# Kernel optimization log

Hardware: AMD Instinct MI355X
Metric: run time of the kernel (lower is better)

## Reference

```python
import jax, jax.numpy as jnp
import numpy as np

B, T, D, W, H = 8, 2048, 1024, 16, 8
HD = D // H  # head dim = 128
EPS = 1e-5


def _layernorm(x, g, b):
    m = jnp.mean(x, axis=-1, keepdims=True)
    v = jnp.var(x, axis=-1, keepdims=True)
    return (x - m) / jnp.sqrt(v + EPS) * g + b


def setup_inputs() -> dict:
    key = jax.random.key(0)
    ks = jax.random.split(key, 8)
    s = 0.02
    return {
        "frame_features": jax.random.normal(ks[0], (B, T, D), dtype=jnp.float32),
        "frame_indices": jnp.arange(B * T, dtype=jnp.int64).reshape(B, T),
        # nn.MultiheadAttention packed in-projection (3D, D) and out projection
        "w_qkv": jax.random.normal(ks[1], (3 * D, D), dtype=jnp.float32) * s,
        "b_qkv": jnp.zeros((3 * D,), dtype=jnp.float32),
        "w_out": jax.random.normal(ks[2], (D, D), dtype=jnp.float32) * s,
        "b_out": jnp.zeros((D,), dtype=jnp.float32),
        # FFN: Linear(D, 4D) -> GELU -> Linear(4D, D)
        "w1": jax.random.normal(ks[3], (4 * D, D), dtype=jnp.float32) * s,
        "b1": jnp.zeros((4 * D,), dtype=jnp.float32),
        "w2": jax.random.normal(ks[4], (D, 4 * D), dtype=jnp.float32) * s,
        "b2": jnp.zeros((D,), dtype=jnp.float32),
        "g1": jnp.ones((D,), dtype=jnp.float32),
        "beta1": jnp.zeros((D,), dtype=jnp.float32),
        "g2": jnp.ones((D,), dtype=jnp.float32),
        "beta2": jnp.zeros((D,), dtype=jnp.float32),
    }


def _forward(frame_features, frame_indices, w_qkv, b_qkv, w_out, b_out,
             w1, b1, w2, b2, g1, beta1, g2, beta2):
    # --- sinusoidal temporal positional encoding, indexed by frame number ---
    pos = frame_indices.astype(jnp.float32)[..., None]          # (B, T, 1)
    div = jnp.exp(-jnp.log(10000.0) * jnp.arange(0, D, 2, dtype=jnp.float32) / D)
    ang = pos * div                                              # (B, T, D/2)
    pe = jnp.stack([jnp.sin(ang), jnp.cos(ang)], axis=-1).reshape(B, T, D)
    x = frame_features + pe

    # --- block-diagonal (local window) attention, all windows in one pass ---
    nw = T // W
    xw = x.reshape(B, nw, W, D)
    qkv = jnp.einsum('bnwd,ed->bnwe', xw, w_qkv) + b_qkv         # (B, nw, W, 3D)
    q, k, v = jnp.split(qkv, 3, axis=-1)
    q = q.reshape(B, nw, W, H, HD)
    k = k.reshape(B, nw, W, H, HD)
    v = v.reshape(B, nw, W, H, HD)
    scores = jnp.einsum('bnqhd,bnkhd->bnhqk', q, k) / jnp.sqrt(jnp.float32(HD))
    attn = jax.nn.softmax(scores, axis=-1)
    o = jnp.einsum('bnhqk,bnkhd->bnqhd', attn, v).reshape(B, nw, W, D)
    attn_out = jnp.einsum('bnwd,ed->bnwe', o, w_out) + b_out

    h = _layernorm(xw + attn_out, g1, beta1)
    ffn = jnp.einsum('bnwf,df->bnwd', jax.nn.gelu(
        jnp.einsum('bnwd,fd->bnwf', h, w1) + b1, approximate=False), w2) + b2
    out = _layernorm(h + ffn, g2, beta2)
    return out.reshape(B, T, D)


def reference(frame_features, frame_indices, w_qkv, b_qkv, w_out, b_out,
              w1, b1, w2, b2, g1, beta1, g2, beta2):
    return _forward(frame_features, frame_indices, w_qkv, b_qkv, w_out, b_out,
                    w1, b1, w2, b2, g1, beta1, g2, beta2)
```

## Files before the change

### kernel.cpp

```cpp
#include <hip/hip_runtime.h>
#include <math.h>

typedef __bf16 bf16;
typedef __bf16 bf16x8 __attribute__((ext_vector_type(8)));
typedef __bf16 bf16x4 __attribute__((ext_vector_type(4)));
typedef __bf16 bf16x2 __attribute__((ext_vector_type(2)));
typedef float f32x4 __attribute__((ext_vector_type(4)));

#define ROWS 16384

typedef __attribute__((address_space(3))) void* lds_vp;
typedef const __attribute__((address_space(1))) void* glb_vp;
__device__ __forceinline__ void gload16(const void* g, void* l) {
  __builtin_amdgcn_global_load_lds((glb_vp)g, (lds_vp)l, 16, 0, 0);
}

__global__ __launch_bounds__(256) void cast4_kernel(
    const float* __restrict__ s0, bf16* __restrict__ d0, int n0,
    const float* __restrict__ s1, bf16* __restrict__ d1, int n1,
    const float* __restrict__ s2, bf16* __restrict__ d2, int n2,
    const float* __restrict__ s3, bf16* __restrict__ d3, int n3)
{
  int i = (blockIdx.x * 256 + threadIdx.x) * 8;
  const float* s; bf16* d;
  if (i < n0)                { s = s0; d = d0; }
  else if ((i -= n0) < n1)   { s = s1; d = d1; }
  else if ((i -= n1) < n2)   { s = s2; d = d2; }
  else if ((i -= n2) < n3)   { s = s3; d = d3; }
  else return;
  float4 a = *(const float4*)(s + i);
  float4 b = *(const float4*)(s + i + 4);
  bf16x8 o;
  o[0] = (bf16)a.x; o[1] = (bf16)a.y; o[2] = (bf16)a.z; o[3] = (bf16)a.w;
  o[4] = (bf16)b.x; o[5] = (bf16)b.y; o[6] = (bf16)b.z; o[7] = (bf16)b.w;
  *(bf16x8*)(d + i) = o;
}

__global__ __launch_bounds__(256) void pe_add_kernel(
    const float* __restrict__ ff, const int* __restrict__ idx, bf16* __restrict__ x)
{
  int p   = blockIdx.x * 256 + threadIdx.x;
  int row = p >> 9;
  int j   = p & 511;
  float pos = (float)idx[row];
  float d2  = (float)(2 * j) * (1.0f / 1024.0f);
  float dv  = expf(-9.210340371976184f * d2);
  float ang = pos * dv;
  float s, c;
  sincosf(ang, &s, &c);
  int base = row * 1024 + 2 * j;
  float2 f = *(const float2*)(ff + base);
  bf16x2 o;
  o[0] = (bf16)(f.x + s);
  o[1] = (bf16)(f.y + c);
  *(bf16x2*)(x + base) = o;
}

#define MFMA16 __builtin_amdgcn_mfma_f32_16x16x32_bf16

template<bool GELU, bool RES>
__global__ __launch_bounds__(512, 2) void gemm8(
    const bf16* __restrict__ A, const bf16* __restrict__ Bw,
    const float* __restrict__ bias, const bf16* __restrict__ resid,
    bf16* __restrict__ C, int M, int N, int K)
{
  extern __shared__ char smem[];

  const int tid  = threadIdx.x;
  const int wave = tid >> 6;
  const int lane = tid & 63;
  const int wm = wave >> 2, wn = wave & 3;
  const int ln = lane & 15, q = lane >> 4;
  const int wm8 = wm * 8, wn4 = wn * 4;

  const int nwg = gridDim.x;
  const int nbn = N >> 8;
  const int swz = (blockIdx.x & 7) * (nwg >> 3) + (blockIdx.x >> 3);
  const int bm = (swz / nbn) << 8;
  const int bn = (swz % nbn) << 8;

  const bf16* lA = (const bf16*)smem;
  const int rsw = (ln * 32 + q * 8) ^ (((ln >> 3) & 1) << 4);
  const int raw = wm8 * 512 + rsw;
  const int rbw = 8192 + wn4 * 512 + rsw;

  const int le = lane ^ (((lane >> 5) & 1) << 1);
  const int sr = le >> 2;
  const int sc = (le & 3) * 8;
  const bf16* gAw = A  + (size_t)(bm + wave * 32 + sr) * K + sc;
  const bf16* gBw = Bw + (size_t)(bn + wave * 32 + sr) * K + sc;

#define STAGE_A(BB, KOFF) do { \
    char* _d = smem + (BB) * 32768 + wave * 2048; \
    gload16(gAw + (KOFF), _d); \
    gload16(gAw + 16 * (size_t)K + (KOFF), _d + 1024); } while (0)
#define STAGE_B(BB, KOFF) do { \
    char* _d = smem + (BB) * 32768 + 16384 + wave * 2048; \
    gload16(gBw + (KOFF), _d); \
    gload16(gBw + 16 * (size_t)K + (KOFF), _d + 1024); } while (0)

  f32x4 acc[8][4];
#pragma unroll
  for (int i = 0; i < 8; i++)
#pragma unroll
    for (int j = 0; j < 4; j++) acc[i][j] = {0.f, 0.f, 0.f, 0.f};

  float bv[4];
#pragma unroll
  for (int tn = 0; tn < 4; tn++) bv[tn] = bias[bn + wn * 64 + tn * 16 + ln];

  const int nkt = K >> 5;

  STAGE_A(0, 0);  STAGE_B(0, 0);
  STAGE_A(1, 32); STAGE_B(1, 32);
  STAGE_A(2, 64); STAGE_B(2, 64);
  asm volatile("s_waitcnt vmcnt(8)");
  __builtin_amdgcn_s_barrier();

#define MFROW(T, AF) \
    acc[T][0] = MFMA16(AF, bf0, acc[T][0], 0, 0, 0); \
    acc[T][1] = MFMA16(AF, bf1, acc[T][1], 0, 0, 0); \
    acc[T][2] = MFMA16(AF, bf2, acc[T][2], 0, 0, 0); \
    acc[T][3] = MFMA16(AF, bf3, acc[T][3], 0, 0, 0);

#define KT(B_, KST, STG, VMS) { \
    if (STG) { STAGE_A((((B_) + 3) & 3), (KST)); STAGE_B((((B_) + 3) & 3), (KST)); } \
    const bf16* _pa = lA + (B_) * 16384 + raw; \
    const bf16* _pb = lA + (B_) * 16384 + rbw; \
    bf16x8 af0 = *(const bf16x8*)(_pa); \
    bf16x8 af1 = *(const bf16x8*)(_pa + 512); \
    bf16x8 af2 = *(const bf16x8*)(_pa + 1024); \
    bf16x8 af3 = *(const bf16x8*)(_pa + 1536); \
    bf16x8 af4 = *(const bf16x8*)(_pa + 2048); \
    bf16x8 af5 = *(const bf16x8*)(_pa + 2560); \
    bf16x8 af6 = *(const bf16x8*)(_pa + 3072); \
    bf16x8 af7 = *(const bf16x8*)(_pa + 3584); \
    bf16x8 bf0 = *(const bf16x8*)(_pb); \
    bf16x8 bf1 = *(const bf16x8*)(_pb + 512); \
    bf16x8 bf2 = *(const bf16x8*)(_pb + 1024); \
    bf16x8 bf3 = *(const bf16x8*)(_pb + 1536); \
    __builtin_amdgcn_s_setprio(1); \
    MFROW(0, af0) MFROW(1, af1) MFROW(2, af2) MFROW(3, af3) \
    MFROW(4, af4) MFROW(5, af5) MFROW(6, af6) MFROW(7, af7) \
    __builtin_amdgcn_s_setprio(0); \
    VMS; \
    __builtin_amdgcn_s_barrier(); }

#define V8 asm volatile("s_waitcnt vmcnt(8)")
#define V4 asm volatile("s_waitcnt vmcnt(4)")
#define V0 asm volatile("s_waitcnt vmcnt(0)")
#define VN (void)0

  for (int mm = 0; mm < nkt - 4; mm += 4) {
    const int kst = (mm + 3) * 32;
    KT(0, kst,       true, V8)
    KT(1, kst + 32,  true, V8)
    KT(2, kst + 64,  true, V8)
    KT(3, kst + 96,  true, V8)
  }
  KT(0, (nkt - 1) * 32, true,  V8)
  KT(1, 0,              false, V4)
  KT(2, 0,              false, V0)
  KT(3, 0,              false, VN)
#undef KT
#undef MFROW
#undef V8
#undef V4
#undef V0
#undef VN
#undef STAGE_A
#undef STAGE_B

  bf16* eb = (bf16*)smem;
  const int lrow = tid >> 4;
  const int cb   = (tid & 15) * 16;
#pragma unroll
  for (int tm = 0; tm < 8; tm++) {
    __syncthreads();
#pragma unroll
    for (int tn = 0; tn < 4; tn++)
#pragma unroll
      for (int i = 0; i < 4; i++)
        eb[(wm * 16 + q * 4 + i) * 264 + wn * 64 + tn * 16 + ln] =
            (bf16)(acc[tm][tn][i] + bv[tn]);
    __syncthreads();
    int gR = bm + (lrow >> 4) * 128 + tm * 16 + (lrow & 15);
    size_t rowoff = (size_t)gR * N + bn + cb;
    bf16x8 v0 = *(const bf16x8*)&eb[lrow * 264 + cb];
    bf16x8 v1 = *(const bf16x8*)&eb[lrow * 264 + cb + 8];
    if (RES) {
      bf16x8 r0 = *(const bf16x8*)(resid + rowoff);
      bf16x8 r1 = *(const bf16x8*)(resid + rowoff + 8);
#pragma unroll
      for (int u = 0; u < 8; u++) {
        v0[u] = (bf16)((float)v0[u] + (float)r0[u]);
        v1[u] = (bf16)((float)v1[u] + (float)r1[u]);
      }
    }
    if (GELU) {
#pragma unroll
      for (int u = 0; u < 8; u++) {
        float a = (float)v0[u], c = (float)v1[u];
        float ea = __builtin_amdgcn_exp2f(2.3022082f * a * (1.0f + 0.044715f * a * a));
        float ec = __builtin_amdgcn_exp2f(2.3022082f * c * (1.0f + 0.044715f * c * c));
        v0[u] = (bf16)(a - a * __builtin_amdgcn_rcpf(ea + 1.0f));
        v1[u] = (bf16)(c - c * __builtin_amdgcn_rcpf(ec + 1.0f));
      }
    }
    *(bf16x8*)(C + rowoff)     = v0;
    *(bf16x8*)(C + rowoff + 8) = v1;
  }
}

__global__ __launch_bounds__(256) void attn_kernel(
    const bf16* __restrict__ qkv, bf16* __restrict__ o)
{
  __shared__ bf16 sq[16][136], sk[16][136], sv[16][136];
  __shared__ float ss[16][17];

  int wid = blockIdx.x;
  int h   = wid & 7;
  int win = wid >> 3;
  int tb  = win * 16;

  int t  = threadIdx.x;
  int r  = t >> 4;
  int c8 = (t & 15) * 8;

  const bf16* base = qkv + (size_t)(tb + r) * 3072 + c8;
  *(bf16x8*)&sq[r][c8] = *(const bf16x8*)(base + h * 128);
  *(bf16x8*)&sk[r][c8] = *(const bf16x8*)(base + 1024 + h * 128);
  *(bf16x8*)&sv[r][c8] = *(const bf16x8*)(base + 2048 + h * 128);
  __syncthreads();

  {
    int i = t >> 4, jj = t & 15;
    float s = 0.f;
#pragma unroll
    for (int d8 = 0; d8 < 16; d8++) {
      bf16x8 qa = *(const bf16x8*)&sq[i][d8 * 8];
      bf16x8 kb = *(const bf16x8*)&sk[jj][d8 * 8];
#pragma unroll
      for (int u = 0; u < 8; u++) s += (float)qa[u] * (float)kb[u];
    }
    ss[i][jj] = s * 0.08838834764831845f;
  }
  __syncthreads();

  if (t < 16) {
    float m = -1e30f;
    for (int jj = 0; jj < 16; jj++) m = fmaxf(m, ss[t][jj]);
    float sum = 0.f;
    for (int jj = 0; jj < 16; jj++) { float e = expf(ss[t][jj] - m); ss[t][jj] = e; sum += e; }
    float inv = 1.0f / sum;
    for (int jj = 0; jj < 16; jj++) ss[t][jj] *= inv;
  }
  __syncthreads();

  {
    int i = t >> 4; int d0 = (t & 15) * 8;
    float acc[8] = {0, 0, 0, 0, 0, 0, 0, 0};
#pragma unroll
    for (int jj = 0; jj < 16; jj++) {
      float a = ss[i][jj];
      bf16x8 vv8 = *(const bf16x8*)&sv[jj][d0];
#pragma unroll
      for (int u = 0; u < 8; u++) acc[u] += a * (float)vv8[u];
    }
    bf16* op = o + (size_t)(tb + i) * 1024 + h * 128 + d0;
    bf16x8 ov;
#pragma unroll
    for (int u = 0; u < 8; u++) ov[u] = (bf16)acc[u];
    *(bf16x8*)op = ov;
  }
}

template<typename OUT_T>
__global__ __launch_bounds__(256) void ln_kernel(
    const bf16* __restrict__ x, const float* __restrict__ g,
    const float* __restrict__ b, OUT_T* __restrict__ y)
{
  __shared__ float red[8];
  int row = blockIdx.x;
  int t   = threadIdx.x;
  int lane = t & 63, wave = t >> 6;

  bf16x4 v4 = *(const bf16x4*)(x + (size_t)row * 1024 + t * 4);
  float v[4];
  float s = 0.f, sq = 0.f;
#pragma unroll
  for (int u = 0; u < 4; u++) {
    v[u] = (float)v4[u];
    s += v[u];
    sq += v[u] * v[u];
  }
  for (int off = 32; off > 0; off >>= 1) {
    s  += __shfl_down(s, off);
    sq += __shfl_down(sq, off);
  }
  if (lane == 0) { red[wave * 2] = s; red[wave * 2 + 1] = sq; }
  __syncthreads();
  float st = red[0] + red[2] + red[4] + red[6];
  float qt = red[1] + red[3] + red[5] + red[7];
  float mean = st * (1.0f / 1024.0f);
  float var  = qt * (1.0f / 1024.0f) - mean * mean;
  float inv  = rsqrtf(var + 1e-5f);
  int c = t * 4;
  OUT_T* yr = y + (size_t)row * 1024 + c;
#pragma unroll
  for (int u = 0; u < 4; u++)
    yr[u] = (OUT_T)((v[u] - mean) * inv * g[c + u] + b[c + u]);
}

extern "C" void kernel_launch(void* const* d_in, const int* in_sizes, int n_in,
                              void* d_out, int out_size, void* d_ws, size_t ws_size,
                              hipStream_t stream) {
  const float* ff    = (const float*)d_in[0];
  const int*   idx   = (const int*)d_in[1];
  const float* w_qkv = (const float*)d_in[2];
  const float* b_qkv = (const float*)d_in[3];
  const float* w_out = (const float*)d_in[4];
  const float* b_out = (const float*)d_in[5];
  const float* w1    = (const float*)d_in[6];
  const float* b1    = (const float*)d_in[7];
  const float* w2    = (const float*)d_in[8];
  const float* b2    = (const float*)d_in[9];
  const float* g1    = (const float*)d_in[10];
  const float* be1   = (const float*)d_in[11];
  const float* g2    = (const float*)d_in[12];
  const float* be2   = (const float*)d_in[13];
  float* out = (float*)d_out;

  static bool attrs_done = false;
  if (!attrs_done) {
    attrs_done = true;
    hipFuncSetAttribute(reinterpret_cast<const void*>(&gemm8<false, false>),
                        hipFuncAttributeMaxDynamicSharedMemorySize, 131072);
    hipFuncSetAttribute(reinterpret_cast<const void*>(&gemm8<false, true>),
                        hipFuncAttributeMaxDynamicSharedMemorySize, 131072);
    hipFuncSetAttribute(reinterpret_cast<const void*>(&gemm8<true, false>),
                        hipFuncAttributeMaxDynamicSharedMemorySize, 131072);
  }

  char* p = (char*)d_ws;
  bf16* x_bf = (bf16*)p;  p += (size_t)ROWS * 1024 * 2;
  bf16* big  = (bf16*)p;  p += (size_t)ROWS * 4096 * 2;
  bf16* s_bf = (bf16*)p;  p += (size_t)ROWS * 1024 * 2;
  bf16* h_bf = (bf16*)p;  p += (size_t)ROWS * 1024 * 2;
  bf16* wqb  = (bf16*)p;  p += (size_t)3072 * 1024 * 2;
  bf16* wob  = (bf16*)p;  p += (size_t)1024 * 1024 * 2;
  bf16* w1b  = (bf16*)p;  p += (size_t)4096 * 1024 * 2;
  bf16* w2b  = (bf16*)p;  p += (size_t)1024 * 4096 * 2;
  bf16* o_bf = big + (size_t)ROWS * 3072;
  bf16* g_bf = big;

  cast4_kernel<<<6144, 256, 0, stream>>>(
      w_qkv, wqb, 3072 * 1024,
      w_out, wob, 1024 * 1024,
      w1,    w1b, 4096 * 1024,
      w2,    w2b, 1024 * 4096);

  pe_add_kernel<<<ROWS * 512 / 256, 256, 0, stream>>>(ff, idx, x_bf);

  gemm8<false, false><<<64 * 12, 512, 131072, stream>>>(
      x_bf, wqb, b_qkv, nullptr, big, ROWS, 3072, 1024);
  attn_kernel<<<(ROWS / 16) * 8, 256, 0, stream>>>(big, o_bf);
  gemm8<false, true><<<64 * 4, 512, 131072, stream>>>(
      o_bf, wob, b_out, x_bf, s_bf, ROWS, 1024, 1024);
  ln_kernel<bf16><<<ROWS, 256, 0, stream>>>(s_bf, g1, be1, h_bf);
  gemm8<true, false><<<64 * 16, 512, 131072, stream>>>(
      h_bf, w1b, b1, nullptr, big, ROWS, 4096, 1024);
  gemm8<false, true><<<64 * 4, 512, 131072, stream>>>(
      g_bf, w2b, b2, h_bf, s_bf, ROWS, 1024, 4096);
  ln_kernel<float><<<ROWS, 256, 0, stream>>>(s_bf, g2, be2, out);
}
```

Before: 657.5 us.

## Replace 4-stage LDS pipeline in GEMM with double buffering to halve shared memory

The GEMM main loop moves from a 4-buffer, 3-deep prefetch pipeline to a 2-buffer ping-pong scheme. Each step now waits for all outstanding loads with vmcnt(0) before the barrier. LDS per block drops from 128KB to 64KB, so the launches request 65536 bytes and the max-dynamic-shared-memory attributes are removed. This can let two 512-thread blocks share a CU, at the cost of a shallower prefetch that exposes more global-load latency per k-step.

```diff
diff --git a/kernel.cpp b/kernel.cpp
--- a/kernel.cpp
+++ b/kernel.cpp
@@ -112,9 +112,7 @@
   const int nkt = K >> 5;
 
   STAGE_A(0, 0);  STAGE_B(0, 0);
-  STAGE_A(1, 32); STAGE_B(1, 32);
-  STAGE_A(2, 64); STAGE_B(2, 64);
-  asm volatile("s_waitcnt vmcnt(8)");
+  asm volatile("s_waitcnt vmcnt(0)");
   __builtin_amdgcn_s_barrier();
 
 #define MFROW(T, AF) \
@@ -123,8 +121,9 @@
     acc[T][2] = MFMA16(AF, bf2, acc[T][2], 0, 0, 0); \
     acc[T][3] = MFMA16(AF, bf3, acc[T][3], 0, 0, 0);
 
-#define KT(B_, KST, STG, VMS) { \
-    if (STG) { STAGE_A((((B_) + 3) & 3), (KST)); STAGE_B((((B_) + 3) & 3), (KST)); } \
+#define KT(B_, NEXT) { \
+    const bool stg = (NEXT) < nkt; \
+    if (stg) { STAGE_A((B_) ^ 1, (NEXT) * 32); STAGE_B((B_) ^ 1, (NEXT) * 32); } \
     const bf16* _pa = lA + (B_) * 16384 + raw; \
     const bf16* _pb = lA + (B_) * 16384 + rbw; \
     bf16x8 af0 = *(const bf16x8*)(_pa); \
@@ -143,31 +142,15 @@
     MFROW(0, af0) MFROW(1, af1) MFROW(2, af2) MFROW(3, af3) \
     MFROW(4, af4) MFROW(5, af5) MFROW(6, af6) MFROW(7, af7) \
     __builtin_amdgcn_s_setprio(0); \
-    VMS; \
+    if (stg) { asm volatile("s_waitcnt vmcnt(0)"); } \
     __builtin_amdgcn_s_barrier(); }
 
-#define V8 asm volatile("s_waitcnt vmcnt(8)")
-#define V4 asm volatile("s_waitcnt vmcnt(4)")
-#define V0 asm volatile("s_waitcnt vmcnt(0)")
-#define VN (void)0
-
-  for (int mm = 0; mm < nkt - 4; mm += 4) {
-    const int kst = (mm + 3) * 32;
-    KT(0, kst,       true, V8)
-    KT(1, kst + 32,  true, V8)
-    KT(2, kst + 64,  true, V8)
-    KT(3, kst + 96,  true, V8)
-  }
-  KT(0, (nkt - 1) * 32, true,  V8)
-  KT(1, 0,              false, V4)
-  KT(2, 0,              false, V0)
-  KT(3, 0,              false, VN)
+  for (int m = 0; m < nkt; m += 2) {
+    KT(0, m + 1)
+    KT(1, m + 2)
+  }
 #undef KT
 #undef MFROW
-#undef V8
-#undef V4
-#undef V0
-#undef VN
 #undef STAGE_A
 #undef STAGE_B
 
@@ -331,17 +314,6 @@
   const float* be2   = (const float*)d_in[13];
   float* out = (float*)d_out;
 
-  static bool attrs_done = false;
-  if (!attrs_done) {
-    attrs_done = true;
-    hipFuncSetAttribute(reinterpret_cast<const void*>(&gemm8<false, false>),
-                        hipFuncAttributeMaxDynamicSharedMemorySize, 131072);
-    hipFuncSetAttribute(reinterpret_cast<const void*>(&gemm8<false, true>),
-                        hipFuncAttributeMaxDynamicSharedMemorySize, 131072);
-    hipFuncSetAttribute(reinterpret_cast<const void*>(&gemm8<true, false>),
-                        hipFuncAttributeMaxDynamicSharedMemorySize, 131072);
-  }
-
   char* p = (char*)d_ws;
   bf16* x_bf = (bf16*)p;  p += (size_t)ROWS * 1024 * 2;
   bf16* big  = (bf16*)p;  p += (size_t)ROWS * 4096 * 2;
@@ -362,15 +334,15 @@
 
   pe_add_kernel<<<ROWS * 512 / 256, 256, 0, stream>>>(ff, idx, x_bf);
 
-  gemm8<false, false><<<64 * 12, 512, 131072, stream>>>(
+  gemm8<false, false><<<64 * 12, 512, 65536, stream>>>(
       x_bf, wqb, b_qkv, nullptr, big, ROWS, 3072, 1024);
   attn_kernel<<<(ROWS / 16) * 8, 256, 0, stream>>>(big, o_bf);
-  gemm8<false, true><<<64 * 4, 512, 131072, stream>>>(
+  gemm8<false, true><<<64 * 4, 512, 65536, stream>>>(
       o_bf, wob, b_out, x_bf, s_bf, ROWS, 1024, 1024);
   ln_kernel<bf16><<<ROWS, 256, 0, stream>>>(s_bf, g1, be1, h_bf);
-  gemm8<true, false><<<64 * 16, 512, 131072, stream>>>(
+  gemm8<true, false><<<64 * 16, 512, 65536, stream>>>(
       h_bf, w1b, b1, nullptr, big, ROWS, 4096, 1024);
-  gemm8<false, true><<<64 * 4, 512, 131072, stream>>>(
+  gemm8<false, true><<<64 * 4, 512, 65536, stream>>>(
       g_bf, w2b, b2, h_bf, s_bf, ROWS, 1024, 4096);
   ln_kernel<float><<<ROWS, 256, 0, stream>>>(s_bf, g2, be2, out);
 }
```

Result: slower. 679.6 us (+3.4%).
